# Performance work log

Measured on AMD Instinct MI355X. Metric: run time of the kernel, lower is better.

## Reference

```python
import jax, jax.numpy as jnp
import numpy as np

# SLAY feature-map hyperparams (must match init_kwargs)
H, D, P, M, R = 4, 128, 16, 32, 2   # heads, head_dim, poly_dim, num_features, quad nodes
EPS = 1e-6
C = 2.0 + EPS
_nodes, _weights = np.polynomial.laguerre.laggauss(R)
QUAD_NODES = jnp.asarray(_nodes, jnp.float32) / C
QUAD_WEIGHTS = jnp.asarray(_weights, jnp.float32) / C

VOCAB, NUM_LABELS, EMBED_DIM = 100000, 32768, 512
B, S, K = 512, 64, 5


def slay_features(x, omega, anchors):
    """SLAY feature map: tensor product of anchored polynomial and PRF features.
    x: [N, EMBED_DIM] -> [N, R*H*P*M]"""
    N = x.shape[0]
    xr = x.reshape(N, H, D)
    xn = xr / jnp.clip(jnp.linalg.norm(xr, axis=-1, keepdims=True), 1e-6)  # safe_normalize
    # anchored polynomial features: [N, H, P]
    poly_feat = jnp.einsum('nhd,pd->nhp', xn, anchors) ** 2 / jnp.sqrt(float(P))
    # positive random features with Gauss-Laguerre quadrature: [R, N, H, M]
    prf_proj = jnp.einsum('nhd,rhdm->rnhm', xn, omega)
    s = QUAD_NODES.reshape(R, 1, 1, 1)
    sqrt_2s = jnp.sqrt(2.0 * jnp.clip(s, 0))
    prf_feat = jnp.exp(jnp.clip(prf_proj * sqrt_2s - s, -10.0, 10.0)) / jnp.sqrt(float(M))
    prf_feat = prf_feat * jnp.sqrt(jnp.clip(QUAD_WEIGHTS.reshape(R, 1, 1, 1), 0))
    # tensor-product fusion: [N, R, H, P, M] -> [N, R*H*P*M]
    fused = jnp.einsum('nhp,rnhm->nrhpm', poly_feat, prf_feat)
    return fused.reshape(N, -1)


def mean_embedding(indices, mask, embedding_table):
    embeds = embedding_table[indices]                       # [B, S, E]
    sum_embeds = jnp.sum(embeds * mask[:, :, None], axis=1)  # [B, E]
    sum_mask = jnp.sum(mask, axis=1, keepdims=True)
    return sum_embeds / jnp.clip(sum_mask, 1e-9)


def setup_inputs() -> dict:
    key = jax.random.key(0)
    k1, k2, k3, k4, k5, k6 = jax.random.split(key, 6)
    indices = jax.random.randint(k1, (B, S), 0, VOCAB)
    mask = jnp.ones((B, S), dtype=jnp.float32)
    labels = jax.random.randint(k2, (B, K), 0, NUM_LABELS)
    label_mask = jnp.ones((B, K), dtype=jnp.float32)
    embedding_table = jax.random.normal(k3, (VOCAB, EMBED_DIM), dtype=jnp.float32) * 0.02
    classifier_kernel = jax.random.normal(k4, (EMBED_DIM, NUM_LABELS), dtype=jnp.float32) * 0.02
    omega = jax.random.normal(k5, (R, H, D, M), dtype=jnp.float32)
    anchors = jax.random.normal(k6, (P, D), dtype=jnp.float32)
    anchors = anchors / jnp.linalg.norm(anchors, axis=-1, keepdims=True)
    return {"indices": indices, "mask": mask, "labels": labels, "label_mask": label_mask,
            "embedding_table": embedding_table, "classifier_kernel": classifier_kernel,
            "omega": omega, "anchors": anchors}


def reference(indices, mask, labels, label_mask, embedding_table, classifier_kernel, omega, anchors):
    query = mean_embedding(indices, mask, embedding_table)            # [B, E]
    phi_query = slay_features(query, omega, anchors)                  # [B, F]
    W_vecs = classifier_kernel.T                                      # [L, E]
    phi_W = slay_features(W_vecs, omega, anchors)                     # [L, F]  (dominant cost)
    Z_approx_vec = jnp.sum(phi_W, axis=0)                             # [F]
    denom = jnp.dot(phi_query, Z_approx_vec) + 1e-6                   # [B]
    log_Z = jnp.log(denom)
    safe_labels = jnp.maximum(labels, 0)
    W_pos = W_vecs[safe_labels]                                       # [B, K, E]
    phi_w_pos = slay_features(W_pos.reshape(-1, EMBED_DIM), omega, anchors).reshape(B, K, -1)
    nums = jnp.sum(phi_w_pos * phi_query[:, None, :], axis=-1) + 1e-6  # [B, K]
    log_probs = jnp.log(nums) - log_Z[:, None]
    loss_total = -jnp.sum(log_probs * label_mask)
    return loss_total / B
```

## Files before the change

kernel.cpp:

```cpp
#include <hip/hip_runtime.h>
#include <math.h>


namespace {
constexpr double Cq  = 2.0 + 1e-6;
constexpr double QN0 = 0.5857864376269049  / Cq;
constexpr double QN1 = 3.414213562373095   / Cq;
constexpr double QW0 = 0.8535533905932738  / Cq;
constexpr double QW1 = 0.14644660940672624 / Cq;

constexpr size_t OFF_QUERY = 0;
constexpr size_t OFF_POLYQ = 262144;
constexpr size_t OFF_PRFQ  = OFF_POLYQ + 32768;
constexpr size_t OFF_Z     = OFF_PRFQ + 131072;
constexpr size_t OFF_LOGZ  = OFF_Z + 4096;
constexpr size_t OFF_ANCT  = OFF_LOGZ + 512;
constexpr size_t OFF_SLOT  = OFF_ANCT + 2048;
constexpr size_t OFF_FEAT  = OFF_SLOT + 32768;
}

__device__ __forceinline__ void accum_feat(const float* __restrict__ x, long xstride,
                                           const float* __restrict__ anct,
                                           const float* __restrict__ omega, int h,
                                           float& sumsq, float poly[16], float prf[64])
{
    for (int d = 0; d < 128; ++d) {
        float xv = x[(long)d * xstride];
        sumsq = fmaf(xv, xv, sumsq);
        const float4* a4 = (const float4*)(anct + d * 16);
#pragma unroll
        for (int j = 0; j < 4; ++j) {
            float4 a = a4[j];
            poly[4*j+0] = fmaf(xv, a.x, poly[4*j+0]);
            poly[4*j+1] = fmaf(xv, a.y, poly[4*j+1]);
            poly[4*j+2] = fmaf(xv, a.z, poly[4*j+2]);
            poly[4*j+3] = fmaf(xv, a.w, poly[4*j+3]);
        }
#pragma unroll
        for (int r = 0; r < 2; ++r) {
            const float4* w4 = (const float4*)(omega + (((r*4 + h)*128 + d) * 32));
#pragma unroll
            for (int j = 0; j < 8; ++j) {
                float4 w = w4[j];
                prf[r*32 + 4*j+0] = fmaf(xv, w.x, prf[r*32 + 4*j+0]);
                prf[r*32 + 4*j+1] = fmaf(xv, w.y, prf[r*32 + 4*j+1]);
                prf[r*32 + 4*j+2] = fmaf(xv, w.z, prf[r*32 + 4*j+2]);
                prf[r*32 + 4*j+3] = fmaf(xv, w.w, prf[r*32 + 4*j+3]);
            }
        }
    }
}

__device__ __forceinline__ void finalize_feat(float sumsq, float poly[16], float prf[64])
{
    float rn = 1.0f / fmaxf(sqrtf(sumsq), 1e-6f);
#pragma unroll
    for (int p = 0; p < 16; ++p) { float v = poly[p] * rn; poly[p] = v * v * 0.25f; }
    const float s0 = (float)QN0, s1 = (float)QN1;
    const float g0 = sqrtf(2.0f * (float)QN0), g1 = sqrtf(2.0f * (float)QN1);
    const float c0 = sqrtf((float)QW0) * 0.17677669529663687f;
    const float c1 = sqrtf((float)QW1) * 0.17677669529663687f;
#pragma unroll
    for (int m = 0; m < 32; ++m) {
        float z0 = prf[m]      * rn * g0 - s0;
        float z1 = prf[32 + m] * rn * g1 - s1;
        z0 = fminf(fmaxf(z0, -10.f), 10.f);
        z1 = fminf(fmaxf(z1, -10.f), 10.f);
        prf[m]      = expf(z0) * c0;
        prf[32 + m] = expf(z1) * c1;
    }
}

__global__ void k_tr_anchors(const float* __restrict__ anchors, float* __restrict__ anct)
{
    for (int i = threadIdx.x; i < 16 * 128; i += 256) {
        int p = i & 15, d = i >> 4;
        anct[i] = anchors[p * 128 + d];
    }
}

__global__ void k_scatter_slots(const int* __restrict__ labels, int* __restrict__ slot)
{
    int i = blockIdx.x * 256 + threadIdx.x;
    if (i < 512 * 5) slot[max(labels[i], 0)] = i;
}

__global__ void k_mean_embed(const int* __restrict__ idx, const float* __restrict__ mask,
                             const float* __restrict__ emb, float* __restrict__ query)
{
    int b = blockIdx.x, t = threadIdx.x;
    float2 acc = make_float2(0.f, 0.f);
    float msum = 0.f;
    for (int s = 0; s < 64; ++s) {
        float mv = mask[b * 64 + s];
        msum += mv;
        const float2* row = (const float2*)(emb + (size_t)idx[b * 64 + s] * 512);
        float2 v = row[t];
        acc.x = fmaf(mv, v.x, acc.x);
        acc.y = fmaf(mv, v.y, acc.y);
    }
    float inv = 1.0f / fmaxf(msum, 1e-9f);
    ((float2*)(query + (size_t)b * 512))[t] = make_float2(acc.x * inv, acc.y * inv);
}

__global__ void k_query_feat(const float* __restrict__ query, const float* __restrict__ anct,
                             const float* __restrict__ omega, float* __restrict__ polyq,
                             float* __restrict__ prfq)
{
    __shared__ float xs[512];
    __shared__ float rnS[4];
    int b = blockIdx.x, t = threadIdx.x;
    xs[t]       = query[(size_t)b * 512 + t];
    xs[t + 256] = query[(size_t)b * 512 + 256 + t];
    __syncthreads();
    int w = t >> 6, lane = t & 63;
    if (w == 0 || w == 1 || w == 2 || w == 3) {
        float v0 = xs[w * 128 + lane], v1 = xs[w * 128 + 64 + lane];
        float ss = fmaf(v0, v0, v1 * v1);
#pragma unroll
        for (int o = 1; o < 64; o <<= 1) ss += __shfl_xor(ss, o, 64);
        if (lane == 0) rnS[w] = 1.0f / fmaxf(sqrtf(ss), 1e-6f);
    }
    __syncthreads();

    const float s_[2] = {(float)QN0, (float)QN1};
    const float g_[2] = {sqrtf(2.0f * (float)QN0), sqrtf(2.0f * (float)QN1)};
    const float c_[2] = {sqrtf((float)QW0) * 0.17677669529663687f,
                         sqrtf((float)QW1) * 0.17677669529663687f};

    for (int tau = t; tau < 320; tau += 256) {
        int h = tau / 80, j = tau - h * 80;
        const float* xh = xs + h * 128;
        float acc = 0.f;
        if (j < 16) {
            for (int d = 0; d < 128; ++d) acc = fmaf(xh[d], anct[d * 16 + j], acc);
            float v = acc * rnS[h];
            polyq[(b * 4 + h) * 16 + j] = v * v * 0.25f;
        } else {
            int rj = j - 16, r = rj >> 5, m = rj & 31;
            const float* om = omega + ((size_t)(r * 4 + h) * 128) * 32 + m;
            for (int d = 0; d < 128; ++d) acc = fmaf(xh[d], om[d * 32], acc);
            float z = acc * rnS[h] * g_[r] - s_[r];
            z = fminf(fmaxf(z, -10.f), 10.f);
            prfq[((b * 2 + r) * 4 + h) * 32 + m] = expf(z) * c_[r];
        }
    }
}

__global__ void __launch_bounds__(256) k_labels(const float* __restrict__ ck,
                                                const float* __restrict__ anct,
                                                const float* __restrict__ omega,
                                                const int* __restrict__ slot,
                                                float* __restrict__ feat,
                                                float* __restrict__ Z)
{
    __shared__ float polyS[128 * 17];
    __shared__ __align__(16) float prfS[128 * 68];
    int t = threadIdx.x;
    int h = blockIdx.x & 3;
    int l = (blockIdx.x >> 2) * 256 + t;

    float sumsq = 0.f, poly[16] = {}, prf[64] = {};
    accum_feat(ck + (size_t)h * 128 * 32768 + l, 32768, anct, omega, h, sumsq, poly, prf);
    finalize_feat(sumsq, poly, prf);

    int s = slot[l];
    if (s >= 0) {
        float4* dst = (float4*)(feat + ((size_t)s * 4 + h) * 80);
#pragma unroll
        for (int j = 0; j < 4; ++j)
            dst[j] = make_float4(poly[4*j], poly[4*j+1], poly[4*j+2], poly[4*j+3]);
#pragma unroll
        for (int j = 0; j < 16; ++j)
            dst[4 + j] = make_float4(prf[4*j], prf[4*j+1], prf[4*j+2], prf[4*j+3]);
    }

    int zr = t >> 7, zp = (t >> 3) & 15, zm4 = t & 7;
    float4 zacc = make_float4(0.f, 0.f, 0.f, 0.f);
#pragma unroll
    for (int bi = 0; bi < 2; ++bi) {
        if ((t >> 7) == bi) {
            int tl = t & 127;
#pragma unroll
            for (int p = 0; p < 16; ++p) polyS[tl * 17 + p] = poly[p];
            float4* dst = (float4*)(prfS + tl * 68);
#pragma unroll
            for (int j = 0; j < 16; ++j)
                dst[j] = make_float4(prf[4*j], prf[4*j+1], prf[4*j+2], prf[4*j+3]);
        }
        __syncthreads();
        for (int q = 0; q < 128; ++q) {
            float  pv = polyS[q * 17 + zp];
            float4 fv = *(const float4*)(prfS + q * 68 + zr * 32 + zm4 * 4);
            zacc.x = fmaf(pv, fv.x, zacc.x);
            zacc.y = fmaf(pv, fv.y, zacc.y);
            zacc.z = fmaf(pv, fv.z, zacc.z);
            zacc.w = fmaf(pv, fv.w, zacc.w);
        }
        __syncthreads();
    }
    float* zdst = Z + ((zr * 4 + h) * 16 + zp) * 32 + zm4 * 4;
    atomicAdd(zdst + 0, zacc.x);
    atomicAdd(zdst + 1, zacc.y);
    atomicAdd(zdst + 2, zacc.z);
    atomicAdd(zdst + 3, zacc.w);
}

__global__ void k_denom(const float* __restrict__ polyq, const float* __restrict__ prfq,
                        const float* __restrict__ Z, float* __restrict__ logZ)
{
    int t = threadIdx.x;
    int lane = t & 63;
    int b = blockIdx.x * 4 + (t >> 6);
    float acc = 0.f;
    for (int i = 0; i < 64; ++i) {
        int f = i * 64 + lane;
        int m = f & 31, p = (f >> 5) & 15, hh = (f >> 9) & 3, r = f >> 11;
        float phi = polyq[(b * 4 + hh) * 16 + p] * prfq[((b * 2 + r) * 4 + hh) * 32 + m];
        acc = fmaf(phi, Z[f], acc);
    }
#pragma unroll
    for (int o = 1; o < 64; o <<= 1) acc += __shfl_xor(acc, o, 64);
    if (lane == 0) logZ[b] = logf(acc + 1e-6f);
}

__global__ void k_loss(const int* __restrict__ labels, const float* __restrict__ lmask,
                       const int* __restrict__ slot, const float* __restrict__ feat,
                       const float* __restrict__ polyq, const float* __restrict__ prfq,
                       const float* __restrict__ logZ, float* __restrict__ out)
{
    int g = blockIdx.x * 256 + threadIdx.x;
    if (g >= 512 * 5 * 4) return;
    int h = g & 3, bk = g >> 2;
    int k = bk % 5, b = bk / 5;
    int l = max(labels[b * 5 + k], 0);
    int s = slot[l];

    const float4* f4 = (const float4*)(feat + ((size_t)s * 4 + h) * 80);
    const float* pq = polyq + (b * 4 + h) * 16;
    const float* q0 = prfq + ((b * 2 + 0) * 4 + h) * 32;
    const float* q1 = prfq + ((b * 2 + 1) * 4 + h) * 32;

    float pd = 0.f;
#pragma unroll
    for (int j = 0; j < 4; ++j) {
        float4 fp = f4[j];
        pd = fmaf(fp.x, pq[4*j+0], pd);
        pd = fmaf(fp.y, pq[4*j+1], pd);
        pd = fmaf(fp.z, pq[4*j+2], pd);
        pd = fmaf(fp.w, pq[4*j+3], pd);
    }
    float f0 = 0.f, f1 = 0.f;
#pragma unroll
    for (int j = 0; j < 8; ++j) {
        float4 fv = f4[4 + j];
        f0 = fmaf(fv.x, q0[4*j+0], f0);
        f0 = fmaf(fv.y, q0[4*j+1], f0);
        f0 = fmaf(fv.z, q0[4*j+2], f0);
        f0 = fmaf(fv.w, q0[4*j+3], f0);
        float4 fw = f4[12 + j];
        f1 = fmaf(fw.x, q1[4*j+0], f1);
        f1 = fmaf(fw.y, q1[4*j+1], f1);
        f1 = fmaf(fw.z, q1[4*j+2], f1);
        f1 = fmaf(fw.w, q1[4*j+3], f1);
    }
    float c = pd * (f0 + f1);
    c += __shfl_xor(c, 1, 64);
    c += __shfl_xor(c, 2, 64);
    if (h == 0) {
        float val = (logf(c + 1e-6f) - logZ[b]) * lmask[b * 5 + k];
        atomicAdd(out, val * (-1.0f / 512.0f));
    }
}

extern "C" void kernel_launch(void* const* d_in, const int* in_sizes, int n_in,
                              void* d_out, int out_size, void* d_ws, size_t ws_size,
                              hipStream_t stream)
{
    const int*   indices = (const int*)  d_in[0];
    const float* mask    = (const float*)d_in[1];
    const int*   labels  = (const int*)  d_in[2];
    const float* lmask   = (const float*)d_in[3];
    const float* emb     = (const float*)d_in[4];
    const float* ck      = (const float*)d_in[5];
    const float* omega   = (const float*)d_in[6];
    const float* anchors = (const float*)d_in[7];
    float* ws  = (float*)d_ws;
    float* out = (float*)d_out;
    int*   slot = (int*)(ws + OFF_SLOT);
    float* feat = ws + OFF_FEAT;

    hipMemsetAsync(ws + OFF_Z, 0, 4096 * sizeof(float), stream);
    hipMemsetAsync(slot, 0xFF, 32768 * sizeof(int), stream);
    hipMemsetAsync(out, 0, sizeof(float), stream);

    k_tr_anchors<<<1, 256, 0, stream>>>(anchors, ws + OFF_ANCT);
    k_scatter_slots<<<10, 256, 0, stream>>>(labels, slot);
    k_mean_embed<<<512, 256, 0, stream>>>(indices, mask, emb, ws + OFF_QUERY);
    k_query_feat<<<512, 256, 0, stream>>>(ws + OFF_QUERY, ws + OFF_ANCT, omega,
                                          ws + OFF_POLYQ, ws + OFF_PRFQ);
    k_labels<<<512, 256, 0, stream>>>(ck, ws + OFF_ANCT, omega, slot, feat, ws + OFF_Z);
    k_denom<<<128, 256, 0, stream>>>(ws + OFF_POLYQ, ws + OFF_PRFQ, ws + OFF_Z,
                                     ws + OFF_LOGZ);
    k_loss<<<40, 256, 0, stream>>>(labels, lmask, slot, feat,
                                   ws + OFF_POLYQ, ws + OFF_PRFQ, ws + OFF_LOGZ, out);
}
```

Before: 414.9 us.

## Fuse setup, embedding, and loss kernels; register-tile Z reduction with in-block combine

Replaces three memsets and two small setup kernels with one single-block setup kernel. The mean-embedding and query-feature kernels become one kernel, so the query no longer goes through global memory. The logZ and loss kernels are merged. In k_labels, the Z accumulation now uses a 4x4 register tile per thread with each wave covering a quarter of the rows, and the waves are reduced in shared memory before the atomics. Launch overhead and per-element work drop, at the cost of higher register use and a serial single-block setup.

New measurement: 460.6 us. 1.11x slower.

```diff
diff --git a/kernel.cpp b/kernel.cpp
--- a/kernel.cpp
+++ b/kernel.cpp
@@ -9,12 +9,10 @@
 constexpr double QW0 = 0.8535533905932738  / Cq;
 constexpr double QW1 = 0.14644660940672624 / Cq;
 
-constexpr size_t OFF_QUERY = 0;
-constexpr size_t OFF_POLYQ = 262144;
-constexpr size_t OFF_PRFQ  = OFF_POLYQ + 32768;
+constexpr size_t OFF_POLYQ = 0;
+constexpr size_t OFF_PRFQ  = 32768;
 constexpr size_t OFF_Z     = OFF_PRFQ + 131072;
-constexpr size_t OFF_LOGZ  = OFF_Z + 4096;
-constexpr size_t OFF_ANCT  = OFF_LOGZ + 512;
+constexpr size_t OFF_ANCT  = OFF_Z + 4096;
 constexpr size_t OFF_SLOT  = OFF_ANCT + 2048;
 constexpr size_t OFF_FEAT  = OFF_SLOT + 32768;
 }
@@ -71,50 +69,49 @@
     }
 }
 
-__global__ void k_tr_anchors(const float* __restrict__ anchors, float* __restrict__ anct)
-{
-    for (int i = threadIdx.x; i < 16 * 128; i += 256) {
+__global__ void k_setup(const float* __restrict__ anchors, const int* __restrict__ labels,
+                        int* __restrict__ slot, float* __restrict__ Z,
+                        float* __restrict__ out, float* __restrict__ anct)
+{
+    int t = threadIdx.x;
+    for (int i = t; i < 32768; i += 1024) slot[i] = -1;
+    for (int i = t; i < 4096; i += 1024) Z[i] = 0.f;
+    if (t == 0) out[0] = 0.f;
+    for (int i = t; i < 2048; i += 1024) {
         int p = i & 15, d = i >> 4;
         anct[i] = anchors[p * 128 + d];
     }
-}
-
-__global__ void k_scatter_slots(const int* __restrict__ labels, int* __restrict__ slot)
-{
-    int i = blockIdx.x * 256 + threadIdx.x;
-    if (i < 512 * 5) slot[max(labels[i], 0)] = i;
-}
-
-__global__ void k_mean_embed(const int* __restrict__ idx, const float* __restrict__ mask,
-                             const float* __restrict__ emb, float* __restrict__ query)
-{
+    __syncthreads();
+    for (int i = t; i < 2560; i += 1024) slot[max(labels[i], 0)] = i;
+}
+
+__global__ void __launch_bounds__(256) k_embed_feat(const int* __restrict__ idx,
+        const float* __restrict__ mask, const float* __restrict__ emb,
+        const float* __restrict__ anct, const float* __restrict__ omega,
+        float* __restrict__ polyq, float* __restrict__ prfq)
+{
+    __shared__ float xs[512];
+    __shared__ float rnS[4];
     int b = blockIdx.x, t = threadIdx.x;
+
     float2 acc = make_float2(0.f, 0.f);
     float msum = 0.f;
+#pragma unroll 8
     for (int s = 0; s < 64; ++s) {
         float mv = mask[b * 64 + s];
-        msum += mv;
         const float2* row = (const float2*)(emb + (size_t)idx[b * 64 + s] * 512);
         float2 v = row[t];
         acc.x = fmaf(mv, v.x, acc.x);
         acc.y = fmaf(mv, v.y, acc.y);
+        msum += mv;
     }
     float inv = 1.0f / fmaxf(msum, 1e-9f);
-    ((float2*)(query + (size_t)b * 512))[t] = make_float2(acc.x * inv, acc.y * inv);
-}
-
-__global__ void k_query_feat(const float* __restrict__ query, const float* __restrict__ anct,
-                             const float* __restrict__ omega, float* __restrict__ polyq,
-                             float* __restrict__ prfq)
-{
-    __shared__ float xs[512];
-    __shared__ float rnS[4];
-    int b = blockIdx.x, t = threadIdx.x;
-    xs[t]       = query[(size_t)b * 512 + t];
-    xs[t + 256] = query[(size_t)b * 512 + 256 + t];
+    xs[2 * t]     = acc.x * inv;
+    xs[2 * t + 1] = acc.y * inv;
     __syncthreads();
+
     int w = t >> 6, lane = t & 63;
-    if (w == 0 || w == 1 || w == 2 || w == 3) {
+    {
         float v0 = xs[w * 128 + lane], v1 = xs[w * 128 + 64 + lane];
         float ss = fmaf(v0, v0, v1 * v1);
 #pragma unroll
@@ -131,16 +128,16 @@
     for (int tau = t; tau < 320; tau += 256) {
         int h = tau / 80, j = tau - h * 80;
         const float* xh = xs + h * 128;
-        float acc = 0.f;
+        float a = 0.f;
         if (j < 16) {
-            for (int d = 0; d < 128; ++d) acc = fmaf(xh[d], anct[d * 16 + j], acc);
-            float v = acc * rnS[h];
+            for (int d = 0; d < 128; ++d) a = fmaf(xh[d], anct[d * 16 + j], a);
+            float v = a * rnS[h];
             polyq[(b * 4 + h) * 16 + j] = v * v * 0.25f;
         } else {
             int rj = j - 16, r = rj >> 5, m = rj & 31;
             const float* om = omega + ((size_t)(r * 4 + h) * 128) * 32 + m;
-            for (int d = 0; d < 128; ++d) acc = fmaf(xh[d], om[d * 32], acc);
-            float z = acc * rnS[h] * g_[r] - s_[r];
+            for (int d = 0; d < 128; ++d) a = fmaf(xh[d], om[d * 32], a);
+            float z = a * rnS[h] * g_[r] - s_[r];
             z = fminf(fmaxf(z, -10.f), 10.f);
             prfq[((b * 2 + r) * 4 + h) * 32 + m] = expf(z) * c_[r];
         }
@@ -154,9 +151,12 @@
                                                 float* __restrict__ feat,
                                                 float* __restrict__ Z)
 {
-    __shared__ float polyS[128 * 17];
-    __shared__ __align__(16) float prfS[128 * 68];
-    int t = threadIdx.x;
+    __shared__ float buf[11264];
+    float* polyS = buf;
+    float* prfS  = buf + 2560;
+    float* Zp    = buf + 2560;
+
+    int t = threadIdx.x, w = t >> 6, lane = t & 63;
     int h = blockIdx.x & 3;
     int l = (blockIdx.x >> 2) * 256 + t;
 
@@ -175,43 +175,77 @@
             dst[4 + j] = make_float4(prf[4*j], prf[4*j+1], prf[4*j+2], prf[4*j+3]);
     }
 
-    int zr = t >> 7, zp = (t >> 3) & 15, zm4 = t & 7;
-    float4 zacc = make_float4(0.f, 0.f, 0.f, 0.f);
+    int r = lane >> 5, p4 = (lane >> 3) & 3, m4 = lane & 7;
+    float zacc[4][4] = {};
+
 #pragma unroll
     for (int bi = 0; bi < 2; ++bi) {
         if ((t >> 7) == bi) {
             int tl = t & 127;
 #pragma unroll
-            for (int p = 0; p < 16; ++p) polyS[tl * 17 + p] = poly[p];
+            for (int p = 0; p < 16; ++p) polyS[tl * 20 + p] = poly[p];
             float4* dst = (float4*)(prfS + tl * 68);
 #pragma unroll
             for (int j = 0; j < 16; ++j)
                 dst[j] = make_float4(prf[4*j], prf[4*j+1], prf[4*j+2], prf[4*j+3]);
         }
         __syncthreads();
-        for (int q = 0; q < 128; ++q) {
-            float  pv = polyS[q * 17 + zp];
-            float4 fv = *(const float4*)(prfS + q * 68 + zr * 32 + zm4 * 4);
-            zacc.x = fmaf(pv, fv.x, zacc.x);
-            zacc.y = fmaf(pv, fv.y, zacc.y);
-            zacc.z = fmaf(pv, fv.z, zacc.z);
-            zacc.w = fmaf(pv, fv.w, zacc.w);
+        int q0 = w * 32;
+        for (int q = 0; q < 32; ++q) {
+            int row = q0 + q;
+            float4 pv = *(const float4*)(polyS + row * 20 + p4 * 4);
+            float4 fv = *(const float4*)(prfS + row * 68 + r * 32 + m4 * 4);
+            zacc[0][0] = fmaf(pv.x, fv.x, zacc[0][0]);
+            zacc[0][1] = fmaf(pv.x, fv.y, zacc[0][1]);
+            zacc[0][2] = fmaf(pv.x, fv.z, zacc[0][2]);
+            zacc[0][3] = fmaf(pv.x, fv.w, zacc[0][3]);
+            zacc[1][0] = fmaf(pv.y, fv.x, zacc[1][0]);
+            zacc[1][1] = fmaf(pv.y, fv.y, zacc[1][1]);
+            zacc[1][2] = fmaf(pv.y, fv.z, zacc[1][2]);
+            zacc[1][3] = fmaf(pv.y, fv.w, zacc[1][3]);
+            zacc[2][0] = fmaf(pv.z, fv.x, zacc[2][0]);
+            zacc[2][1] = fmaf(pv.z, fv.y, zacc[2][1]);
+            zacc[2][2] = fmaf(pv.z, fv.z, zacc[2][2]);
+            zacc[2][3] = fmaf(pv.z, fv.w, zacc[2][3]);
+            zacc[3][0] = fmaf(pv.w, fv.x, zacc[3][0]);
+            zacc[3][1] = fmaf(pv.w, fv.y, zacc[3][1]);
+            zacc[3][2] = fmaf(pv.w, fv.z, zacc[3][2]);
+            zacc[3][3] = fmaf(pv.w, fv.w, zacc[3][3]);
         }
         __syncthreads();
     }
-    float* zdst = Z + ((zr * 4 + h) * 16 + zp) * 32 + zm4 * 4;
-    atomicAdd(zdst + 0, zacc.x);
-    atomicAdd(zdst + 1, zacc.y);
-    atomicAdd(zdst + 2, zacc.z);
-    atomicAdd(zdst + 3, zacc.w);
-}
-
-__global__ void k_denom(const float* __restrict__ polyq, const float* __restrict__ prfq,
-                        const float* __restrict__ Z, float* __restrict__ logZ)
-{
-    int t = threadIdx.x;
-    int lane = t & 63;
+
+#pragma unroll
+    for (int i = 0; i < 4; ++i) {
+        float* zp = Zp + w * 1024 + (r * 16 + p4 * 4 + i) * 32 + m4 * 4;
+        *(float4*)zp = make_float4(zacc[i][0], zacc[i][1], zacc[i][2], zacc[i][3]);
+    }
+    __syncthreads();
+
+    int f = t * 4;
+    float4 a0 = *(const float4*)(Zp + f);
+    float4 a1 = *(const float4*)(Zp + 1024 + f);
+    float4 a2 = *(const float4*)(Zp + 2048 + f);
+    float4 a3 = *(const float4*)(Zp + 3072 + f);
+    float sx = a0.x + a1.x + a2.x + a3.x;
+    float sy = a0.y + a1.y + a2.y + a3.y;
+    float sz = a0.z + a1.z + a2.z + a3.z;
+    float sw = a0.w + a1.w + a2.w + a3.w;
+    float* zdst = Z + (f >> 9) * 2048 + h * 512 + (f & 511);
+    atomicAdd(zdst + 0, sx);
+    atomicAdd(zdst + 1, sy);
+    atomicAdd(zdst + 2, sz);
+    atomicAdd(zdst + 3, sw);
+}
+
+__global__ void k_final(const float* __restrict__ polyq, const float* __restrict__ prfq,
+                        const float* __restrict__ Z, const int* __restrict__ labels,
+                        const float* __restrict__ lmask, const int* __restrict__ slot,
+                        const float* __restrict__ feat, float* __restrict__ out)
+{
+    int t = threadIdx.x, lane = t & 63;
     int b = blockIdx.x * 4 + (t >> 6);
+
     float acc = 0.f;
     for (int i = 0; i < 64; ++i) {
         int f = i * 64 + lane;
@@ -221,55 +255,47 @@
     }
 #pragma unroll
     for (int o = 1; o < 64; o <<= 1) acc += __shfl_xor(acc, o, 64);
-    if (lane == 0) logZ[b] = logf(acc + 1e-6f);
-}
-
-__global__ void k_loss(const int* __restrict__ labels, const float* __restrict__ lmask,
-                       const int* __restrict__ slot, const float* __restrict__ feat,
-                       const float* __restrict__ polyq, const float* __restrict__ prfq,
-                       const float* __restrict__ logZ, float* __restrict__ out)
-{
-    int g = blockIdx.x * 256 + threadIdx.x;
-    if (g >= 512 * 5 * 4) return;
-    int h = g & 3, bk = g >> 2;
-    int k = bk % 5, b = bk / 5;
-    int l = max(labels[b * 5 + k], 0);
-    int s = slot[l];
-
-    const float4* f4 = (const float4*)(feat + ((size_t)s * 4 + h) * 80);
-    const float* pq = polyq + (b * 4 + h) * 16;
-    const float* q0 = prfq + ((b * 2 + 0) * 4 + h) * 32;
-    const float* q1 = prfq + ((b * 2 + 1) * 4 + h) * 32;
-
-    float pd = 0.f;
-#pragma unroll
-    for (int j = 0; j < 4; ++j) {
-        float4 fp = f4[j];
-        pd = fmaf(fp.x, pq[4*j+0], pd);
-        pd = fmaf(fp.y, pq[4*j+1], pd);
-        pd = fmaf(fp.z, pq[4*j+2], pd);
-        pd = fmaf(fp.w, pq[4*j+3], pd);
-    }
-    float f0 = 0.f, f1 = 0.f;
-#pragma unroll
-    for (int j = 0; j < 8; ++j) {
-        float4 fv = f4[4 + j];
-        f0 = fmaf(fv.x, q0[4*j+0], f0);
-        f0 = fmaf(fv.y, q0[4*j+1], f0);
-        f0 = fmaf(fv.z, q0[4*j+2], f0);
-        f0 = fmaf(fv.w, q0[4*j+3], f0);
-        float4 fw = f4[12 + j];
-        f1 = fmaf(fw.x, q1[4*j+0], f1);
-        f1 = fmaf(fw.y, q1[4*j+1], f1);
-        f1 = fmaf(fw.z, q1[4*j+2], f1);
-        f1 = fmaf(fw.w, q1[4*j+3], f1);
-    }
-    float c = pd * (f0 + f1);
-    c += __shfl_xor(c, 1, 64);
-    c += __shfl_xor(c, 2, 64);
-    if (h == 0) {
-        float val = (logf(c + 1e-6f) - logZ[b]) * lmask[b * 5 + k];
-        atomicAdd(out, val * (-1.0f / 512.0f));
+    float logZb = logf(acc + 1e-6f);
+
+    if (lane < 20) {
+        int k = lane >> 2, h = lane & 3;
+        int l = max(labels[b * 5 + k], 0);
+        int s = slot[l];
+        const float4* f4 = (const float4*)(feat + ((size_t)s * 4 + h) * 80);
+        const float* pq = polyq + (b * 4 + h) * 16;
+        const float* q0 = prfq + ((b * 2 + 0) * 4 + h) * 32;
+        const float* q1 = prfq + ((b * 2 + 1) * 4 + h) * 32;
+
+        float pd = 0.f;
+#pragma unroll
+        for (int j = 0; j < 4; ++j) {
+            float4 fp = f4[j];
+            pd = fmaf(fp.x, pq[4*j+0], pd);
+            pd = fmaf(fp.y, pq[4*j+1], pd);
+            pd = fmaf(fp.z, pq[4*j+2], pd);
+            pd = fmaf(fp.w, pq[4*j+3], pd);
+        }
+        float f0 = 0.f, f1 = 0.f;
+#pragma unroll
+        for (int j = 0; j < 8; ++j) {
+            float4 fv = f4[4 + j];
+            f0 = fmaf(fv.x, q0[4*j+0], f0);
+            f0 = fmaf(fv.y, q0[4*j+1], f0);
+            f0 = fmaf(fv.z, q0[4*j+2], f0);
+            f0 = fmaf(fv.w, q0[4*j+3], f0);
+            float4 fw = f4[12 + j];
+            f1 = fmaf(fw.x, q1[4*j+0], f1);
+            f1 = fmaf(fw.y, q1[4*j+1], f1);
+            f1 = fmaf(fw.z, q1[4*j+2], f1);
+            f1 = fmaf(fw.w, q1[4*j+3], f1);
+        }
+        float c = pd * (f0 + f1);
+        c += __shfl_xor(c, 1, 64);
+        c += __shfl_xor(c, 2, 64);
+        if (h == 0) {
+            float val = (logf(c + 1e-6f) - logZb) * lmask[b * 5 + k];
+            atomicAdd(out, val * (-1.0f / 512.0f));
+        }
     }
 }
 
@@ -290,18 +316,10 @@
     int*   slot = (int*)(ws + OFF_SLOT);
     float* feat = ws + OFF_FEAT;
 
-    hipMemsetAsync(ws + OFF_Z, 0, 4096 * sizeof(float), stream);
-    hipMemsetAsync(slot, 0xFF, 32768 * sizeof(int), stream);
-    hipMemsetAsync(out, 0, sizeof(float), stream);
-
-    k_tr_anchors<<<1, 256, 0, stream>>>(anchors, ws + OFF_ANCT);
-    k_scatter_slots<<<10, 256, 0, stream>>>(labels, slot);
-    k_mean_embed<<<512, 256, 0, stream>>>(indices, mask, emb, ws + OFF_QUERY);
-    k_query_feat<<<512, 256, 0, stream>>>(ws + OFF_QUERY, ws + OFF_ANCT, omega,
+    k_setup<<<1, 1024, 0, stream>>>(anchors, labels, slot, ws + OFF_Z, out, ws + OFF_ANCT);
+    k_embed_feat<<<512, 256, 0, stream>>>(indices, mask, emb, ws + OFF_ANCT, omega,
                                           ws + OFF_POLYQ, ws + OFF_PRFQ);
     k_labels<<<512, 256, 0, stream>>>(ck, ws + OFF_ANCT, omega, slot, feat, ws + OFF_Z);
-    k_denom<<<128, 256, 0, stream>>>(ws + OFF_POLYQ, ws + OFF_PRFQ, ws + OFF_Z,
-                                     ws + OFF_LOGZ);
-    k_loss<<<40, 256, 0, stream>>>(labels, lmask, slot, feat,
-                                   ws + OFF_POLYQ, ws + OFF_PRFQ, ws + OFF_LOGZ, out);
-}
+    k_final<<<128, 256, 0, stream>>>(ws + OFF_POLYQ, ws + OFF_PRFQ, ws + OFF_Z,
+                                     labels, lmask, slot, feat, out);
+}
```
